# Optimization experiments

Hardware: AMD Instinct MI355X
Metric: run time of the kernel (lower is better)

The kernel has to match this reference:

```python
import jax, jax.numpy as jnp
import numpy as np

B, E, F = 16384, 128, 6
ITEM_V, CATE_V, HIST = 91718, 11, 50
I_IDX, J_IDX = np.triu_indices(F, k=1)  # 15 field pairs, loop order (0,1),(0,2),...
EPS = 1e-5


def _xavier(key, shape):
    fan_in, fan_out = shape[0], shape[-1]
    std = (2.0 / (fan_in + fan_out)) ** 0.5
    return std * jax.random.normal(key, shape, dtype=jnp.float32)


def setup_inputs() -> dict:
    key = jax.random.key(0)
    ks = jax.random.split(key, 20)
    inp = {
        'item_id': jax.random.randint(ks[0], (B,), 0, ITEM_V),
        'item_emb_d128': jax.random.normal(ks[1], (B, 128), dtype=jnp.float32),
        'likes_level': jax.random.randint(ks[2], (B,), 0, CATE_V),
        'views_level': jax.random.randint(ks[3], (B,), 0, CATE_V),
        'item_seq': jax.random.randint(ks[4], (B, HIST), 0, ITEM_V),
        # learned parameters
        'item_emb': 0.05 * jax.random.normal(ks[5], (ITEM_V, E), dtype=jnp.float32),
        'cate_emb': 0.05 * jax.random.normal(ks[6], (CATE_V, E), dtype=jnp.float32),
        'mm_W': _xavier(ks[7], (128, E)), 'mm_b': jnp.zeros((E,), jnp.float32),
        'ln_g': jnp.ones((E,), jnp.float32), 'ln_b': jnp.zeros((E,), jnp.float32),
        'se_W1': _xavier(ks[8], (F, F // 2)), 'se_b1': jnp.zeros((F // 2,), jnp.float32),
        'se_W2': _xavier(ks[9], (F // 2, F)), 'se_b2': jnp.zeros((F,), jnp.float32),
        'bi_W': _xavier(ks[10], (E, E)),
        'mlp_W1': _xavier(ks[11], (21 * E, 512)), 'mlp_b1': jnp.zeros((512,), jnp.float32),
        'bn1_g': jnp.ones((512,), jnp.float32), 'bn1_b': jnp.zeros((512,), jnp.float32),
        'bn1_rm': jnp.zeros((512,), jnp.float32), 'bn1_rv': jnp.ones((512,), jnp.float32),
        'mlp_W2': _xavier(ks[12], (512, 256)), 'mlp_b2': jnp.zeros((256,), jnp.float32),
        'bn2_g': jnp.ones((256,), jnp.float32), 'bn2_b': jnp.zeros((256,), jnp.float32),
        'bn2_rm': jnp.zeros((256,), jnp.float32), 'bn2_rv': jnp.ones((256,), jnp.float32),
        'mlp_W3': _xavier(ks[13], (256, 1)), 'mlp_b3': jnp.zeros((1,), jnp.float32),
    }
    return inp


def _forward(item_id, item_emb_d128, likes_level, views_level, item_seq,
             item_emb, cate_emb, mm_W, mm_b, ln_g, ln_b,
             se_W1, se_b1, se_W2, se_b2, bi_W,
             mlp_W1, mlp_b1, bn1_g, bn1_b, bn1_rm, bn1_rv,
             mlp_W2, mlp_b2, bn2_g, bn2_b, bn2_rm, bn2_rv,
             mlp_W3, mlp_b3):
    b = item_id.shape[0]
    tab = item_emb.at[0].set(0.0)  # padding_idx=0
    like_feat = cate_emb[likes_level]
    view_feat = cate_emb[views_level]
    item_feat = tab[item_id]
    # mm_proj: Linear -> LayerNorm -> ReLU
    mm = item_emb_d128 @ mm_W + mm_b
    mu = mm.mean(-1, keepdims=True)
    var = jnp.var(mm, axis=-1, keepdims=True)
    mm = jax.nn.relu((mm - mu) / jnp.sqrt(var + EPS) * ln_g + ln_b)
    # masked mean pooling over history
    seq_emb = tab[item_seq]                               # (B, HIST, E)
    valid = (item_seq != 0).astype(seq_emb.dtype)
    seq_sum = (seq_emb * valid[..., None]).sum(1)
    cnt = jnp.clip(valid.sum(1, keepdims=True), 1.0)
    hist_feat = seq_sum / cnt
    user_feat = jnp.zeros((b, E), seq_emb.dtype)
    x = jnp.stack([user_feat, like_feat, view_feat, item_feat, mm, hist_feat], axis=1)  # (B,6,E)
    # SENet
    z = x.mean(-1)
    w = jax.nn.sigmoid(jax.nn.relu(z @ se_W1 + se_b1) @ se_W2 + se_b2)
    xs = x * w[:, :, None]
    # bilinear 'all'
    xw = jnp.einsum('bfe,ed->bfd', xs, bi_W)
    p = xs[:, I_IDX, :] * xw[:, J_IDX, :]                 # (B,15,E)
    c = jnp.concatenate([xs.reshape(b, -1), p.reshape(b, -1)], axis=1)  # (B, 2688)
    # MLP head (eval mode: BN uses running stats, dropout off)
    h = c @ mlp_W1 + mlp_b1
    h = jax.nn.relu((h - bn1_rm) / jnp.sqrt(bn1_rv + EPS) * bn1_g + bn1_b)
    h = h @ mlp_W2 + mlp_b2
    h = jax.nn.relu((h - bn2_rm) / jnp.sqrt(bn2_rv + EPS) * bn2_g + bn2_b)
    logits = h @ mlp_W3 + mlp_b3
    return jax.nn.sigmoid(logits)[:, 0]


def reference(item_id, item_emb_d128, likes_level, views_level, item_seq,
              item_emb, cate_emb, mm_W, mm_b, ln_g, ln_b,
              se_W1, se_b1, se_W2, se_b2, bi_W,
              mlp_W1, mlp_b1, bn1_g, bn1_b, bn1_rm, bn1_rv,
              mlp_W2, mlp_b2, bn2_g, bn2_b, bn2_rm, bn2_rv,
              mlp_W3, mlp_b3):
    return _forward(item_id, item_emb_d128, likes_level, views_level, item_seq,
                    item_emb, cate_emb, mm_W, mm_b, ln_g, ln_b,
                    se_W1, se_b1, se_W2, se_b2, bi_W,
                    mlp_W1, mlp_b1, bn1_g, bn1_b, bn1_rm, bn1_rv,
                    mlp_W2, mlp_b2, bn2_g, bn2_b, bn2_rm, bn2_rv,
                    mlp_W3, mlp_b3)
```

## Files before the change

kernel.cpp:

```cpp
#include <hip/hip_runtime.h>
#include <hip/hip_bf16.h>

typedef __hip_bfloat16 bfloat;
typedef __bf16 bf16x8 __attribute__((ext_vector_type(8)));
typedef float f32x4 __attribute__((ext_vector_type(4)));

#define B_SZ   16384
#define E_DIM  128
#define HIST_L 50


__device__ __constant__ int ISL[10] = {0,0,0,0,1,1,1,2,2,3};

__device__ __forceinline__ void gl_lds16(const void* g, void* l) {
    __builtin_amdgcn_global_load_lds(
        (const __attribute__((address_space(1))) unsigned int*)g,
        (__attribute__((address_space(3))) unsigned int*)l, 16, 0, 0);
}

template<int TB>
__global__ __launch_bounds__(256) void feat_kernel(
    const int* __restrict__ item_id,
    const int* __restrict__ likes, const int* __restrict__ views,
    const int* __restrict__ seq,
    const void* __restrict__ item_tab, const float* __restrict__ cate_emb,
    const float* __restrict__ d128, const bfloat* __restrict__ mmWt,
    const float* __restrict__ mm_b,
    const float* __restrict__ ln_g, const float* __restrict__ ln_b,
    const float* __restrict__ se_W1, const float* __restrict__ se_b1,
    const float* __restrict__ se_W2, const float* __restrict__ se_b2,
    bfloat* __restrict__ xs)
{
    const int tid = threadIdx.x;
    const int r   = tid >> 7;
    const int e   = tid & 127;
    const int b   = blockIdx.x * 2 + r;
    const int w   = tid >> 6;

    __shared__ float redh[2][4][128];
    __shared__ float d128s[2][128];
    __shared__ int   seq_s[2][64];
    __shared__ float lnred[4], lnred2[4];
    __shared__ float zred[5][4];
    __shared__ float wsh[2][6];
    __shared__ int   cnt_s[2];

    if (e < 64) seq_s[r][e] = (e < HIST_L) ? seq[(size_t)b * HIST_L + e] : 0;
    d128s[r][e] = d128[(size_t)b * 128 + e];
    __syncthreads();

    const int iid = item_id[b];
    const float like_v = cate_emb[likes[b] * 128 + e];
    const float view_v = cate_emb[views[b] * 128 + e];
    float item_v;
    if (TB) {
        const bfloat* tb = (const bfloat*)item_tab;
        item_v = __bfloat162float(tb[(size_t)iid * 128 + e]);
    } else {
        const float* tf = (const float*)item_tab;
        float raw = tf[(size_t)iid * 128 + e];
        item_v = iid ? raw : 0.f;
    }

    const int q   = e >> 5;
    const int l32 = e & 31;
    float4 hs = make_float4(0.f, 0.f, 0.f, 0.f);
    if (TB) {
        const ushort* tb = (const ushort*)item_tab;
        #pragma unroll
        for (int g = 0; g < 13; ++g) {
            int s = seq_s[r][g * 4 + q];
            ushort4 v = *(const ushort4*)&tb[(size_t)s * 128 + l32 * 4];
            hs.x += __bfloat162float(__ushort_as_bfloat16(v.x));
            hs.y += __bfloat162float(__ushort_as_bfloat16(v.y));
            hs.z += __bfloat162float(__ushort_as_bfloat16(v.z));
            hs.w += __bfloat162float(__ushort_as_bfloat16(v.w));
        }
    } else {
        const float* tf = (const float*)item_tab;
        #pragma unroll
        for (int g = 0; g < 13; ++g) {
            int s = seq_s[r][g * 4 + q];
            const float4 v = *(const float4*)&tf[(size_t)s * 128 + l32 * 4];
            float m = (s != 0) ? 1.f : 0.f;
            hs.x = fmaf(v.x, m, hs.x);
            hs.y = fmaf(v.y, m, hs.y);
            hs.z = fmaf(v.z, m, hs.z);
            hs.w = fmaf(v.w, m, hs.w);
        }
    }

    float acc = mm_b[e];
    {
        const ushort* wrow = (const ushort*)(mmWt + (size_t)e * 128);
        #pragma unroll
        for (int k8 = 0; k8 < 16; ++k8) {
            union { bf16x8 v; ushort s[8]; } u;
            u.v = *(const bf16x8*)&wrow[k8 * 8];
            const float* dp = &d128s[r][k8 * 8];
            #pragma unroll
            for (int j = 0; j < 8; ++j)
                acc = fmaf(dp[j],
                           __bfloat162float(__ushort_as_bfloat16(u.s[j])),
                           acc);
        }
    }

    {
        float v = acc;
        #pragma unroll
        for (int off = 32; off > 0; off >>= 1) v += __shfl_down(v, off, 64);
        if ((tid & 63) == 0) lnred[w] = v;
    }
    __syncthreads();
    const float mu = (lnred[2 * r] + lnred[2 * r + 1]) * (1.f / 128.f);
    const float d  = acc - mu;
    {
        float v = d * d;
        #pragma unroll
        for (int off = 32; off > 0; off >>= 1) v += __shfl_down(v, off, 64);
        if ((tid & 63) == 0) lnred2[w] = v;
    }
    redh[r][q][l32 * 4 + 0] = hs.x;
    redh[r][q][l32 * 4 + 1] = hs.y;
    redh[r][q][l32 * 4 + 2] = hs.z;
    redh[r][q][l32 * 4 + 3] = hs.w;
    if ((w & 1) == 0 && e < 64) {
        bool valid = (e < HIST_L) && (seq_s[r][e] != 0);
        unsigned long long m = __ballot(valid);
        if (e == 0) cnt_s[r] = (int)__popcll(m);
    }
    __syncthreads();
    const float var = (lnred2[2 * r] + lnred2[2 * r + 1]) * (1.f / 128.f);
    float xmm = d * rsqrtf(var + 1e-5f) * ln_g[e] + ln_b[e];
    xmm = fmaxf(xmm, 0.f);

    const int cnt = cnt_s[r] > 0 ? cnt_s[r] : 1;
    const float hist_v = (redh[r][0][e] + redh[r][1][e] +
                          redh[r][2][e] + redh[r][3][e]) / (float)cnt;

    {
        float s1 = like_v, s2 = view_v, s3 = item_v, s4 = xmm, s5 = hist_v;
        #pragma unroll
        for (int off = 32; off > 0; off >>= 1) {
            s1 += __shfl_down(s1, off, 64);
            s2 += __shfl_down(s2, off, 64);
            s3 += __shfl_down(s3, off, 64);
            s4 += __shfl_down(s4, off, 64);
            s5 += __shfl_down(s5, off, 64);
        }
        if ((tid & 63) == 0) {
            zred[0][w] = s1; zred[1][w] = s2; zred[2][w] = s3;
            zred[3][w] = s4; zred[4][w] = s5;
        }
    }
    __syncthreads();

    if (e == 0) {
        float z[6];
        z[0] = 0.f;
        #pragma unroll
        for (int f = 1; f < 6; ++f)
            z[f] = (zred[f - 1][2 * r] + zred[f - 1][2 * r + 1]) * (1.f / 128.f);
        float a[3];
        #pragma unroll
        for (int j = 0; j < 3; ++j) {
            float s = se_b1[j];
            #pragma unroll
            for (int f = 0; f < 6; ++f) s += z[f] * se_W1[f * 3 + j];
            a[j] = fmaxf(s, 0.f);
        }
        #pragma unroll
        for (int f = 0; f < 6; ++f) {
            float s = se_b2[f];
            #pragma unroll
            for (int j = 0; j < 3; ++j) s += a[j] * se_W2[j * 6 + f];
            wsh[r][f] = 1.f / (1.f + expf(-s));
        }
    }
    __syncthreads();

    bfloat* xrow = xs + (size_t)b * 640;
    xrow[0 * 128 + e] = __float2bfloat16(like_v * wsh[r][1]);
    xrow[1 * 128 + e] = __float2bfloat16(view_v * wsh[r][2]);
    xrow[2 * 128 + e] = __float2bfloat16(item_v * wsh[r][3]);
    xrow[3 * 128 + e] = __float2bfloat16(xmm    * wsh[r][4]);
    xrow[4 * 128 + e] = __float2bfloat16(hist_v * wsh[r][5]);
}

__global__ __launch_bounds__(256) void mega_prep(
    const float* __restrict__ W1, bfloat* __restrict__ W1t,
    const float* __restrict__ W2, const float* __restrict__ bi_W,
    const float* __restrict__ mm_W,
    bfloat* __restrict__ W2t, bfloat* __restrict__ bWt,
    bfloat* __restrict__ mmWt,
    const float* __restrict__ lb1, const float* __restrict__ g1,
    const float* __restrict__ bb1, const float* __restrict__ rm1,
    const float* __restrict__ rv1,
    const float* __restrict__ lb2, const float* __restrict__ g2,
    const float* __restrict__ bb2, const float* __restrict__ rm2,
    const float* __restrict__ rv2,
    float* __restrict__ S1, float* __restrict__ T1,
    float* __restrict__ S2, float* __restrict__ T2,
    const float* __restrict__ item_emb, bfloat* __restrict__ itemb)
{
    const int blk = blockIdx.x;
    const int tid = threadIdx.x;
    if (blk < 240) {
        __shared__ float t[64][65];
        const int kk0 = (blk % 30) * 64, n0 = (blk / 30) * 64;
        const int j = tid & 63;
        #pragma unroll
        for (int p = 0; p < 16; ++p) {
            int i = (tid >> 6) + p * 4;
            int kk = kk0 + i;
            int orig = kk + (kk < 640 ? 128 : 768);
            t[i][j] = W1[(size_t)orig * 512 + n0 + j];
        }
        __syncthreads();
        #pragma unroll
        for (int p = 0; p < 16; ++p) {
            int i = (tid >> 6) + p * 4;
            W1t[(size_t)(n0 + i) * 1920 + kk0 + j] = __float2bfloat16(t[j][i]);
        }
    } else if (blk < 884) {
        int idx = (blk - 240) * 256 + tid;
        if (idx < 131072) {
            int k = idx >> 8, n = idx & 255;
            W2t[(size_t)n * 512 + k] = __float2bfloat16(W2[idx]);
        } else if (idx < 147456) {
            int t2 = idx - 131072;
            int k = t2 >> 7, n = t2 & 127;
            bWt[n * 128 + k] = __float2bfloat16(bi_W[t2]);
        } else if (idx < 163840) {
            int t2 = idx - 147456;
            int k = t2 >> 7, n = t2 & 127;
            mmWt[n * 128 + k] = __float2bfloat16(mm_W[t2]);
        } else if (idx < 164352) {
            int j = idx - 163840;
            float s = g1[j] * rsqrtf(rv1[j] + 1e-5f);
            S1[j] = s;
            T1[j] = (lb1[j] - rm1[j]) * s + bb1[j];
        } else if (idx < 164608) {
            int j = idx - 164352;
            float s = g2[j] * rsqrtf(rv2[j] + 1e-5f);
            S2[j] = s;
            T2[j] = (lb2[j] - rm2[j]) * s + bb2[j];
        }
    } else {
        if (itemb == nullptr) return;
        const int n8 = 91718 * 128 / 8;
        int idx = (blk - 884) * 256 + tid;
        if (idx >= n8) return;
        if (idx < 16) {
            union { bf16x8 v; unsigned short s[8]; } z;
            #pragma unroll
            for (int i = 0; i < 8; ++i) z.s[i] = 0;
            ((bf16x8*)itemb)[idx] = z.v;
            return;
        }
        float4 f0 = ((const float4*)item_emb)[idx * 2];
        float4 f1 = ((const float4*)item_emb)[idx * 2 + 1];
        union { bf16x8 v; unsigned short s[8]; } u;
        u.s[0] = __bfloat16_as_ushort(__float2bfloat16(f0.x));
        u.s[1] = __bfloat16_as_ushort(__float2bfloat16(f0.y));
        u.s[2] = __bfloat16_as_ushort(__float2bfloat16(f0.z));
        u.s[3] = __bfloat16_as_ushort(__float2bfloat16(f0.w));
        u.s[4] = __bfloat16_as_ushort(__float2bfloat16(f1.x));
        u.s[5] = __bfloat16_as_ushort(__float2bfloat16(f1.y));
        u.s[6] = __bfloat16_as_ushort(__float2bfloat16(f1.z));
        u.s[7] = __bfloat16_as_ushort(__float2bfloat16(f1.w));
        ((bf16x8*)itemb)[idx] = u.v;
    }
}

__global__ __launch_bounds__(256, 1) void gemm_mlp1(
    const bfloat* __restrict__ Axs, const bfloat* __restrict__ Ap,
    const bfloat* __restrict__ Bt, bfloat* __restrict__ C,
    int M, int N, int K,
    const float* __restrict__ S, const float* __restrict__ T)
{
    extern __shared__ __align__(16) short smem[];

    const int tid  = threadIdx.x;
    const int bm   = blockIdx.x * 256;
    const int bn   = blockIdx.y * 128;
    const int wave = tid >> 6;
    const int lane = tid & 63;
    const int wm   = (wave >> 1) * 128;
    const int wn   = (wave & 1) * 64;

    const short* Ag  = (const short*)Axs;
    const short* A2g = (const short*)Ap;
    const short* Bg  = (const short*)Bt;

    f32x4 acc[8][4];
    #pragma unroll
    for (int i = 0; i < 8; ++i)
        #pragma unroll
        for (int j = 0; j < 4; ++j)
            acc[i][j] = (f32x4){0.f, 0.f, 0.f, 0.f};

    const int l8  = lane >> 3;
    const int gch = (lane & 7) ^ l8;

    auto stage = [&](int buf, int kt) {
        short* Ab = smem + buf * 24576;
        short* Bb = Ab + 16384;
        #pragma unroll
        for (int d = 0; d < 4; ++d) {
            int seg = wave * 4 + d;
            int row = seg * 8 + l8;
            gl_lds16(&Bg[(long)(bn + row) * K + kt + gch * 8],
                     &Bb[seg * 512 + lane * 8]);
        }
        #pragma unroll
        for (int d = 0; d < 8; ++d) {
            int seg = wave * 8 + d;
            int row = seg * 8 + l8;
            long rb = (long)(bm + row);
            const short* src = (kt < 640)
                ? &Ag [rb * 640  + kt + gch * 8]
                : &A2g[rb * 1280 + (kt - 640) + gch * 8];
            gl_lds16(src, &Ab[seg * 512 + lane * 8]);
        }
    };

    const int rbase = lane & 15;
    const int rsw   = rbase & 7;

    const int nk = K >> 6;
    stage(0, 0);
    stage(1, 64);

    for (int i = 0; i < nk; ++i) {
        if (i + 1 < nk) asm volatile("s_waitcnt vmcnt(12)" ::: "memory");
        else            asm volatile("s_waitcnt vmcnt(0)" ::: "memory");
        __builtin_amdgcn_s_barrier();
        __builtin_amdgcn_sched_barrier(0);

        if (i + 2 < nk) stage((i + 2) % 3, (i + 2) << 6);

        const short* Ab = smem + (i % 3) * 24576;
        const short* Bb = Ab + 16384;
        #pragma unroll
        for (int h = 0; h < 2; ++h) {
            const int cg = h * 4 + (lane >> 4);
            const int ca = (cg ^ rsw) << 3;
            bf16x8 af[8], bfr[4];
            #pragma unroll
            for (int mt = 0; mt < 8; ++mt)
                af[mt] = *(const bf16x8*)
                    &Ab[(wm + mt * 16 + rbase) * 64 + ca];
            #pragma unroll
            for (int nt = 0; nt < 4; ++nt)
                bfr[nt] = *(const bf16x8*)
                    &Bb[(wn + nt * 16 + rbase) * 64 + ca];
            #pragma unroll
            for (int mt = 0; mt < 8; ++mt)
                #pragma unroll
                for (int nt = 0; nt < 4; ++nt)
                    acc[mt][nt] = __builtin_amdgcn_mfma_f32_16x16x32_bf16(
                        af[mt], bfr[nt], acc[mt][nt], 0, 0, 0);
        }
    }

    const int col0 = lane & 15;
    const int row0 = (lane >> 4) * 4;
    #pragma unroll
    for (int nt = 0; nt < 4; ++nt) {
        int col = bn + wn + nt * 16 + col0;
        float s = S[col], t = T[col];
        #pragma unroll
        for (int mt = 0; mt < 8; ++mt) {
            #pragma unroll
            for (int i = 0; i < 4; ++i) {
                int row = bm + wm + mt * 16 + row0 + i;
                float v = fmaxf(acc[mt][nt][i] * s + t, 0.f);
                C[(size_t)row * N + col] = __float2bfloat16(v);
            }
        }
    }
}

template<int MODE, int EPI, int F32OUT>
__global__ __launch_bounds__(256, 2) void gemm_bt(
    const void* __restrict__ A, const bfloat* __restrict__ A2,
    const bfloat* __restrict__ Bt, void* __restrict__ C,
    int M, int N, int K,
    const float* __restrict__ S, const float* __restrict__ T)
{
    __shared__ __align__(16) short As[4][128 * 32];
    __shared__ __align__(16) short Bs[4][128 * 32];

    const int tid  = threadIdx.x;
    const int bm   = blockIdx.x * 128;
    const int bn   = blockIdx.y * 128;
    const int wave = tid >> 6;
    const int lane = tid & 63;
    const int wm   = (wave >> 1) * 64;
    const int wn   = (wave & 1) * 64;

    const short* Ag  = (const short*)A;
    const short* Bg  = (const short*)Bt;

    f32x4 acc[4][4];
    #pragma unroll
    for (int i = 0; i < 4; ++i)
        #pragma unroll
        for (int j = 0; j < 4; ++j)
            acc[i][j] = (f32x4){0.f, 0.f, 0.f, 0.f};

    const int srow = tid >> 2;
    const int sck  = tid & 3;

    auto stage = [&](int buf, int kt) {
        #pragma unroll
        for (int rr = 0; rr < 2; ++rr) {
            int row = srow + rr * 64;
            int g   = sck ^ ((row >> 1) & 3);
            gl_lds16(&Bg[(long)(bn + row) * K + kt + g * 8],
                     &Bs[buf][row * 32 + sck * 8]);
        }
        #pragma unroll
        for (int rr = 0; rr < 2; ++rr) {
            int row = srow + rr * 64;
            int g   = sck ^ ((row >> 1) & 3);
            const short* src;
            if (MODE == 2) {
                int gr = bm + row;
                src = &Ag[((long)(gr >> 2)) * 640 +
                          ((gr & 3) + 1) * 128 + kt + g * 8];
            } else {
                src = &Ag[(long)(bm + row) * K + kt + g * 8];
            }
            gl_lds16(src, &As[buf][row * 32 + sck * 8]);
        }
    };

    const int rbase = lane & 15;
    const int cg    = lane >> 4;
    const int ca    = (cg ^ ((rbase >> 1) & 3)) << 3;

    const int nk = K >> 5;
    stage(0, 0);
    stage(1, 32);
    if (nk > 2) stage(2, 64);

    for (int i = 0; i < nk; ++i) {
        if (i + 2 < nk)
            asm volatile("s_waitcnt vmcnt(8)" ::: "memory");
        else if (i + 1 < nk)
            asm volatile("s_waitcnt vmcnt(4)" ::: "memory");
        else
            asm volatile("s_waitcnt vmcnt(0)" ::: "memory");
        __builtin_amdgcn_s_barrier();
        __builtin_amdgcn_sched_barrier(0);

        const int cur = i & 3;
        bf16x8 af[4], bfr[4];
        #pragma unroll
        for (int mt = 0; mt < 4; ++mt)
            af[mt] = *(const bf16x8*)
                &As[cur][(wm + mt * 16 + rbase) * 32 + ca];
        #pragma unroll
        for (int nt = 0; nt < 4; ++nt)
            bfr[nt] = *(const bf16x8*)
                &Bs[cur][(wn + nt * 16 + rbase) * 32 + ca];
        #pragma unroll
        for (int mt = 0; mt < 4; ++mt)
            #pragma unroll
            for (int nt = 0; nt < 4; ++nt)
                acc[mt][nt] = __builtin_amdgcn_mfma_f32_16x16x32_bf16(
                    af[mt], bfr[nt], acc[mt][nt], 0, 0, 0);

        if (i + 3 < nk) stage((i + 3) & 3, (i + 3) << 5);
    }

    const int col0 = lane & 15;
    const int row0 = (lane >> 4) * 4;
    #pragma unroll
    for (int nt = 0; nt < 4; ++nt) {
        int col = bn + wn + nt * 16 + col0;
        float s = 1.f, t = 0.f;
        if (EPI == 1 || EPI == 2) { s = (EPI == 1) ? S[col] : 1.f; t = T[col]; }
        #pragma unroll
        for (int mt = 0; mt < 4; ++mt) {
            #pragma unroll
            for (int i = 0; i < 4; ++i) {
                int row = bm + wm + mt * 16 + row0 + i;
                float v = acc[mt][nt][i];
                if (EPI == 3) {
                    const bfloat* xsp = (const bfloat*)A;
                    bfloat* Pp = (bfloat*)C;
                    long b = row >> 2;
                    int pplist[4];
                    int npp;
                    if (i == 0)      { npp = 1; pplist[0] = 0; }
                    else if (i == 1) { npp = 2; pplist[0] = 1; pplist[1] = 4; }
                    else if (i == 2) { npp = 3; pplist[0] = 2; pplist[1] = 5; pplist[2] = 7; }
                    else             { npp = 4; pplist[0] = 3; pplist[1] = 6; pplist[2] = 8; pplist[3] = 9; }
                    #pragma unroll
                    for (int t2 = 0; t2 < npp; ++t2) {
                        int pp  = pplist[t2];
                        int isl = ISL[pp];
                        float xv = __bfloat162float(
                            xsp[b * 640 + isl * 128 + col]);
                        Pp[b * 1280 + pp * 128 + col] =
                            __float2bfloat16(xv * v);
                    }
                } else {
                    if (EPI == 1) v = fmaxf(v * s + t, 0.f);
                    if (EPI == 2) v = v + t;
                    if (F32OUT) ((float*)C)[(size_t)row * N + col] = v;
                    else ((bfloat*)C)[(size_t)row * N + col] = __float2bfloat16(v);
                }
            }
        }
    }
}

__global__ __launch_bounds__(256) void head_kernel(
    const bfloat* __restrict__ h2, const float* __restrict__ W3,
    const float* __restrict__ b3, float* __restrict__ out)
{
    int lane = threadIdx.x & 63;
    int row  = blockIdx.x * 4 + (threadIdx.x >> 6);
    float acc = 0.f;
    #pragma unroll
    for (int i = 0; i < 4; ++i)
        acc += __bfloat162float(h2[(size_t)row * 256 + i * 64 + lane]) *
               W3[i * 64 + lane];
    #pragma unroll
    for (int off = 32; off > 0; off >>= 1) acc += __shfl_down(acc, off, 64);
    if (lane == 0) {
        float l = acc + b3[0];
        out[row] = 1.f / (1.f + expf(-l));
    }
}

extern "C" void kernel_launch(void* const* d_in, const int* in_sizes, int n_in,
                              void* d_out, int out_size, void* d_ws, size_t ws_size,
                              hipStream_t stream) {
    const int*   item_id = (const int*)  d_in[0];
    const float* d128    = (const float*)d_in[1];
    const int*   likes   = (const int*)  d_in[2];
    const int*   views   = (const int*)  d_in[3];
    const int*   seq     = (const int*)  d_in[4];
    const float* item_emb= (const float*)d_in[5];
    const float* cate_emb= (const float*)d_in[6];
    const float* mm_W    = (const float*)d_in[7];
    const float* mm_b    = (const float*)d_in[8];
    const float* ln_g    = (const float*)d_in[9];
    const float* ln_b    = (const float*)d_in[10];
    const float* se_W1   = (const float*)d_in[11];
    const float* se_b1   = (const float*)d_in[12];
    const float* se_W2   = (const float*)d_in[13];
    const float* se_b2   = (const float*)d_in[14];
    const float* bi_W    = (const float*)d_in[15];
    const float* W1      = (const float*)d_in[16];
    const float* b1      = (const float*)d_in[17];
    const float* bn1_g   = (const float*)d_in[18];
    const float* bn1_b   = (const float*)d_in[19];
    const float* bn1_rm  = (const float*)d_in[20];
    const float* bn1_rv  = (const float*)d_in[21];
    const float* W2      = (const float*)d_in[22];
    const float* b2      = (const float*)d_in[23];
    const float* bn2_g   = (const float*)d_in[24];
    const float* bn2_b   = (const float*)d_in[25];
    const float* bn2_rm  = (const float*)d_in[26];
    const float* bn2_rv  = (const float*)d_in[27];
    const float* W3      = (const float*)d_in[28];
    const float* b3      = (const float*)d_in[29];

    const size_t fixed = 2300416;
    const size_t ITB   = 23479808;
    int CH; bool use_tb;
    if      (fixed + ITB + (size_t)16384 * 4864 <= ws_size) { CH = 16384; use_tb = true;  }
    else if (fixed + (size_t)16384 * 4864 <= ws_size)       { CH = 16384; use_tb = false; }
    else if (fixed + ITB + (size_t)8192 * 4864 <= ws_size)  { CH = 8192;  use_tb = true;  }
    else if (fixed + (size_t)8192 * 4864 <= ws_size)        { CH = 8192;  use_tb = false; }
    else if (fixed + ITB + (size_t)4096 * 4864 <= ws_size)  { CH = 4096;  use_tb = true;  }
    else if (fixed + (size_t)4096 * 4864 <= ws_size)        { CH = 4096;  use_tb = false; }
    else if (fixed + (size_t)2048 * 4864 <= ws_size)        { CH = 2048;  use_tb = false; }
    else                                                    { CH = 1024;  use_tb = false; }

    char* ws = (char*)d_ws;
    bfloat* W1t = (bfloat*)(ws);
    bfloat* W2t = (bfloat*)(ws + 1966080);
    bfloat* bWt = (bfloat*)(ws + 2228224);
    bfloat* mmWt= (bfloat*)(ws + 2260992);
    float*  S1  = (float*) (ws + 2293760);
    float*  T1  = (float*) (ws + 2295808);
    float*  S2  = (float*) (ws + 2297856);
    float*  T2  = (float*) (ws + 2298880);
    bfloat* itemb = (bfloat*)(ws + fixed);
    char*   cb  = ws + fixed + (use_tb ? ITB : 0);
    bfloat* xs  = (bfloat*)(cb);
    bfloat* h1  = (bfloat*)(cb + (size_t)CH * 1280);
    bfloat* P   = (bfloat*)(cb + (size_t)CH * 2304);
    bfloat* h2  = (bfloat*)P;

    {
        int nblk = 884 + (use_tb ? (91718 * 128 / 8 + 255) / 256 : 0);
        mega_prep<<<nblk, 256, 0, stream>>>(
            W1, W1t, W2, bi_W, mm_W, W2t, bWt, mmWt,
            b1, bn1_g, bn1_b, bn1_rm, bn1_rv,
            b2, bn2_g, bn2_b, bn2_rm, bn2_rv,
            S1, T1, S2, T2,
            item_emb, use_tb ? itemb : nullptr);
    }

    for (int off = 0; off < B_SZ; off += CH) {
        if (use_tb)
            feat_kernel<1><<<CH / 2, 256, 0, stream>>>(
                item_id + off, likes + off, views + off,
                seq + (size_t)off * HIST_L, itemb, cate_emb,
                d128 + (size_t)off * 128, mmWt, mm_b,
                ln_g, ln_b, se_W1, se_b1, se_W2, se_b2, xs);
        else
            feat_kernel<0><<<CH / 2, 256, 0, stream>>>(
                item_id + off, likes + off, views + off,
                seq + (size_t)off * HIST_L, item_emb, cate_emb,
                d128 + (size_t)off * 128, mmWt, mm_b,
                ln_g, ln_b, se_W1, se_b1, se_W2, se_b2, xs);

        dim3 gxw(CH * 4 / 128, 1);
        gemm_bt<2, 3, 0><<<gxw, 256, 0, stream>>>(
            xs, nullptr, bWt, P, CH * 4, 128, 128, nullptr, nullptr);

        dim3 g1(CH / 256, 4);
        gemm_mlp1<<<g1, 256, 147456, stream>>>(
            xs, P, W1t, h1, CH, 512, 1920, S1, T1);

        dim3 g2(CH / 128, 2);
        gemm_bt<0, 1, 0><<<g2, 256, 0, stream>>>(
            h1, nullptr, W2t, h2, CH, 256, 512, S2, T2);

        head_kernel<<<CH / 4, 256, 0, stream>>>(h2, W3, b3, (float*)d_out + off);
    }
}
```

Baseline: 315.8 us.

## Move multimodal projection out of feature kernel into an MFMA GEMM

Replaces the per-thread scalar FMA loop in feat_kernel, which computed the d128 x mm_W projection, with a separate bf16 matrix-core GEMM launch. The prep kernel now converts d128 to bf16 and copies mm_b into a bias buffer, and feat_kernel reads the precomputed fp32 projection. This removes roughly 128 FMAs per element and the weight-row reads from the gather-bound feature kernel. In exchange it adds an extra launch, an extra pass converting d128 to bf16, and a round trip of the projection through global memory, and it rounds d128 to bf16.

```diff
diff --git a/kernel.cpp b/kernel.cpp
--- a/kernel.cpp
+++ b/kernel.cpp
@@ -24,8 +24,7 @@
     const int* __restrict__ likes, const int* __restrict__ views,
     const int* __restrict__ seq,
     const void* __restrict__ item_tab, const float* __restrict__ cate_emb,
-    const float* __restrict__ d128, const bfloat* __restrict__ mmWt,
-    const float* __restrict__ mm_b,
+    const float* __restrict__ mm,
     const float* __restrict__ ln_g, const float* __restrict__ ln_b,
     const float* __restrict__ se_W1, const float* __restrict__ se_b1,
     const float* __restrict__ se_W2, const float* __restrict__ se_b2,
@@ -38,7 +37,6 @@
     const int w   = tid >> 6;
 
     __shared__ float redh[2][4][128];
-    __shared__ float d128s[2][128];
     __shared__ int   seq_s[2][64];
     __shared__ float lnred[4], lnred2[4];
     __shared__ float zred[5][4];
@@ -46,7 +44,6 @@
     __shared__ int   cnt_s[2];
 
     if (e < 64) seq_s[r][e] = (e < HIST_L) ? seq[(size_t)b * HIST_L + e] : 0;
-    d128s[r][e] = d128[(size_t)b * 128 + e];
     __syncthreads();
 
     const int iid = item_id[b];
@@ -61,6 +58,7 @@
         float raw = tf[(size_t)iid * 128 + e];
         item_v = iid ? raw : 0.f;
     }
+    const float acc = mm[(size_t)b * 128 + e];
 
     const int q   = e >> 5;
     const int l32 = e & 31;
@@ -87,22 +85,6 @@
             hs.y = fmaf(v.y, m, hs.y);
             hs.z = fmaf(v.z, m, hs.z);
             hs.w = fmaf(v.w, m, hs.w);
-        }
-    }
-
-    float acc = mm_b[e];
-    {
-        const ushort* wrow = (const ushort*)(mmWt + (size_t)e * 128);
-        #pragma unroll
-        for (int k8 = 0; k8 < 16; ++k8) {
-            union { bf16x8 v; ushort s[8]; } u;
-            u.v = *(const bf16x8*)&wrow[k8 * 8];
-            const float* dp = &d128s[r][k8 * 8];
-            #pragma unroll
-            for (int j = 0; j < 8; ++j)
-                acc = fmaf(dp[j],
-                           __bfloat162float(__ushort_as_bfloat16(u.s[j])),
-                           acc);
         }
     }
 
@@ -200,8 +182,11 @@
     const float* __restrict__ lb2, const float* __restrict__ g2,
     const float* __restrict__ bb2, const float* __restrict__ rm2,
     const float* __restrict__ rv2,
+    const float* __restrict__ mm_b,
     float* __restrict__ S1, float* __restrict__ T1,
     float* __restrict__ S2, float* __restrict__ T2,
+    float* __restrict__ Tmm,
+    const float* __restrict__ d128, bfloat* __restrict__ d128b,
     const float* __restrict__ item_emb, bfloat* __restrict__ itemb)
 {
     const int blk = blockIdx.x;
@@ -246,11 +231,27 @@
             float s = g2[j] * rsqrtf(rv2[j] + 1e-5f);
             S2[j] = s;
             T2[j] = (lb2[j] - rm2[j]) * s + bb2[j];
-        }
+        } else if (idx < 164736) {
+            Tmm[idx - 164608] = mm_b[idx - 164608];
+        }
+    } else if (blk < 1908) {
+        int idx = (blk - 884) * 256 + tid;
+        float4 f0 = ((const float4*)d128)[idx * 2];
+        float4 f1 = ((const float4*)d128)[idx * 2 + 1];
+        union { bf16x8 v; unsigned short s[8]; } u;
+        u.s[0] = __bfloat16_as_ushort(__float2bfloat16(f0.x));
+        u.s[1] = __bfloat16_as_ushort(__float2bfloat16(f0.y));
+        u.s[2] = __bfloat16_as_ushort(__float2bfloat16(f0.z));
+        u.s[3] = __bfloat16_as_ushort(__float2bfloat16(f0.w));
+        u.s[4] = __bfloat16_as_ushort(__float2bfloat16(f1.x));
+        u.s[5] = __bfloat16_as_ushort(__float2bfloat16(f1.y));
+        u.s[6] = __bfloat16_as_ushort(__float2bfloat16(f1.z));
+        u.s[7] = __bfloat16_as_ushort(__float2bfloat16(f1.w));
+        ((bf16x8*)d128b)[idx] = u.v;
     } else {
         if (itemb == nullptr) return;
         const int n8 = 91718 * 128 / 8;
-        int idx = (blk - 884) * 256 + tid;
+        int idx = (blk - 1908) * 256 + tid;
         if (idx >= n8) return;
         if (idx < 16) {
             union { bf16x8 v; unsigned short s[8]; } z;
@@ -574,16 +575,17 @@
     const float* b3      = (const float*)d_in[29];
 
     const size_t fixed = 2300416;
+    const size_t DB    = 4194304;
     const size_t ITB   = 23479808;
     int CH; bool use_tb;
-    if      (fixed + ITB + (size_t)16384 * 4864 <= ws_size) { CH = 16384; use_tb = true;  }
-    else if (fixed + (size_t)16384 * 4864 <= ws_size)       { CH = 16384; use_tb = false; }
-    else if (fixed + ITB + (size_t)8192 * 4864 <= ws_size)  { CH = 8192;  use_tb = true;  }
-    else if (fixed + (size_t)8192 * 4864 <= ws_size)        { CH = 8192;  use_tb = false; }
-    else if (fixed + ITB + (size_t)4096 * 4864 <= ws_size)  { CH = 4096;  use_tb = true;  }
-    else if (fixed + (size_t)4096 * 4864 <= ws_size)        { CH = 4096;  use_tb = false; }
-    else if (fixed + (size_t)2048 * 4864 <= ws_size)        { CH = 2048;  use_tb = false; }
-    else                                                    { CH = 1024;  use_tb = false; }
+    if      (fixed + DB + ITB + (size_t)16384 * 4864 <= ws_size) { CH = 16384; use_tb = true;  }
+    else if (fixed + DB + (size_t)16384 * 4864 <= ws_size)       { CH = 16384; use_tb = false; }
+    else if (fixed + DB + ITB + (size_t)8192 * 4864 <= ws_size)  { CH = 8192;  use_tb = true;  }
+    else if (fixed + DB + (size_t)8192 * 4864 <= ws_size)        { CH = 8192;  use_tb = false; }
+    else if (fixed + DB + ITB + (size_t)4096 * 4864 <= ws_size)  { CH = 4096;  use_tb = true;  }
+    else if (fixed + DB + (size_t)4096 * 4864 <= ws_size)        { CH = 4096;  use_tb = false; }
+    else if (fixed + DB + (size_t)2048 * 4864 <= ws_size)        { CH = 2048;  use_tb = false; }
+    else                                                         { CH = 1024;  use_tb = false; }
 
     char* ws = (char*)d_ws;
     bfloat* W1t = (bfloat*)(ws);
@@ -594,35 +596,42 @@
     float*  T1  = (float*) (ws + 2295808);
     float*  S2  = (float*) (ws + 2297856);
     float*  T2  = (float*) (ws + 2298880);
-    bfloat* itemb = (bfloat*)(ws + fixed);
-    char*   cb  = ws + fixed + (use_tb ? ITB : 0);
+    float*  Tmm = (float*) (ws + 2299904);
+    bfloat* d128b = (bfloat*)(ws + fixed);
+    bfloat* itemb = (bfloat*)(ws + fixed + DB);
+    char*   cb  = ws + fixed + DB + (use_tb ? ITB : 0);
     bfloat* xs  = (bfloat*)(cb);
     bfloat* h1  = (bfloat*)(cb + (size_t)CH * 1280);
     bfloat* P   = (bfloat*)(cb + (size_t)CH * 2304);
+    float*  mm  = (float*)P;
     bfloat* h2  = (bfloat*)P;
 
     {
-        int nblk = 884 + (use_tb ? (91718 * 128 / 8 + 255) / 256 : 0);
+        int nblk = 1908 + (use_tb ? (91718 * 128 / 8 + 255) / 256 : 0);
         mega_prep<<<nblk, 256, 0, stream>>>(
             W1, W1t, W2, bi_W, mm_W, W2t, bWt, mmWt,
             b1, bn1_g, bn1_b, bn1_rm, bn1_rv,
             b2, bn2_g, bn2_b, bn2_rm, bn2_rv,
-            S1, T1, S2, T2,
+            mm_b, S1, T1, S2, T2, Tmm,
+            d128, d128b,
             item_emb, use_tb ? itemb : nullptr);
     }
 
     for (int off = 0; off < B_SZ; off += CH) {
+        dim3 gmm(CH / 128, 1);
+        gemm_bt<0, 2, 1><<<gmm, 256, 0, stream>>>(
+            d128b + (size_t)off * 128, nullptr, mmWt, mm,
+            CH, 128, 128, nullptr, Tmm);
+
         if (use_tb)
             feat_kernel<1><<<CH / 2, 256, 0, stream>>>(
                 item_id + off, likes + off, views + off,
-                seq + (size_t)off * HIST_L, itemb, cate_emb,
-                d128 + (size_t)off * 128, mmWt, mm_b,
+                seq + (size_t)off * HIST_L, itemb, cate_emb, mm,
                 ln_g, ln_b, se_W1, se_b1, se_W2, se_b2, xs);
         else
             feat_kernel<0><<<CH / 2, 256, 0, stream>>>(
                 item_id + off, likes + off, views + off,
-                seq + (size_t)off * HIST_L, item_emb, cate_emb,
-                d128 + (size_t)off * 128, mmWt, mm_b,
+                seq + (size_t)off * HIST_L, item_emb, cate_emb, mm,
                 ln_g, ln_b, se_W1, se_b1, se_W2, se_b2, xs);
 
         dim3 gxw(CH * 4 / 128, 1);
```

Result: faster. 271.6 us (-14.0%).
